# Performance work log

Hardware: AMD Instinct MI355X
Metric: run time of the kernel (lower is better)

Reference implementation:

```python
import jax, jax.numpy as jnp
import numpy as np
import math

D = 768
H = 12
DH = D // H
L = 2
EPS = 1e-12
NEG = -10000.0


def layer_norm(x, w, b):
    u = jnp.mean(x, axis=-1, keepdims=True)
    s = jnp.mean((x - u) ** 2, axis=-1, keepdims=True)
    return w * ((x - u) / jnp.sqrt(s + EPS)) + b


def mha(q_in, k_in, v_in, mask, qw, qb, kw, kb, vw, vb):
    # q_in: (B,Lq,D); k_in/v_in: (B,Lk,D); mask: (B,Lq,Lk) or (B,1,Lk)
    B, Lq, _ = q_in.shape
    def proj(x, w, b):
        y = x @ w.T + b
        return y.reshape(x.shape[0], x.shape[1], H, DH).transpose(0, 2, 1, 3)
    q = proj(q_in, qw, qb)  # (B,H,Lq,DH)
    k = proj(k_in, kw, kb)
    v = proj(v_in, vw, vb)
    scores = jnp.einsum('bhqd,bhkd->bhqk', q, k) / math.sqrt(DH)
    scores = scores + (1.0 - mask[:, None]) * NEG  # additive mask, (B,1,Lq,Lk) broadcast
    probs = jax.nn.softmax(scores, axis=-1)
    ctx = jnp.einsum('bhqk,bhkd->bhqd', probs, v)
    return ctx.transpose(0, 2, 1, 3).reshape(B, Lq, D)


def setup_inputs() -> dict:
    key = jax.random.key(0)
    ks = jax.random.split(key, 8)
    B, Lt, Lv = 8, 1024, 512
    inp = {
        'dec_hidden_states': jax.random.normal(ks[0], (B, Lt, D), jnp.float32),
        'dec_mask': jnp.ones((B, Lt), jnp.float32),
        'enc_outputs': jax.random.normal(ks[1], (B, Lv, D), jnp.float32),
        'enc_mask': jnp.ones((B, Lv), jnp.float32),
    }
    wkeys = jax.random.split(ks[2], 7)
    names = ['sa_qw', 'sa_kw', 'sa_vw', 'ca_qw', 'ca_kw', 'ca_vw', 'out_w']
    for n, k in zip(names, wkeys):
        inp[n] = 0.02 * jax.random.normal(k, (L, D, D), jnp.float32)
    for n in ['sa_qb', 'sa_kb', 'sa_vb', 'ca_qb', 'ca_kb', 'ca_vb', 'out_b', 'n1_b', 'n2_b', 'n3_b']:
        inp[n] = jnp.zeros((L, D), jnp.float32)
    for n in ['n1_w', 'n2_w', 'n3_w']:
        inp[n] = jnp.ones((L, D), jnp.float32)
    return inp


def reference(dec_hidden_states, dec_mask, enc_outputs, enc_mask,
              sa_qw, sa_qb, sa_kw, sa_kb, sa_vw, sa_vb, n1_w, n1_b,
              ca_qw, ca_qb, ca_kw, ca_kb, ca_vw, ca_vb, n2_w, n2_b,
              out_w, out_b, n3_w, n3_b):
    Lt = dec_hidden_states.shape[1]
    causal = jnp.tril(jnp.ones((Lt, Lt), dec_mask.dtype))
    self_mask = dec_mask[:, None, :] * causal[None]        # (B,Lt,Lt)
    cross_mask = enc_mask[:, None, :]                      # (B,1,Lv)

    params = (sa_qw, sa_qb, sa_kw, sa_kb, sa_vw, sa_vb, n1_w, n1_b,
              ca_qw, ca_qb, ca_kw, ca_kb, ca_vw, ca_vb, n2_w, n2_b,
              out_w, out_b, n3_w, n3_b)

    def body(x, p):
        (qw, qb, kw, kb, vw, vb, w1, b1,
         cqw, cqb, ckw, ckb, cvw, cvb, w2, b2,
         ow, ob, w3, b3) = p
        a = mha(x, x, x, self_mask, qw, qb, kw, kb, vw, vb)
        x1 = layer_norm(a + x, w1, b1)
        c = mha(x1, enc_outputs, enc_outputs, cross_mask, cqw, cqb, ckw, ckb, cvw, cvb)
        x2 = layer_norm(x1 + c, w2, b2)
        # BertOutput called with (x2, x2): LN(dense(x2) + x2)
        y = layer_norm(x2 @ ow.T + ob + x2, w3, b3)
        return y, None

    out, _ = jax.lax.scan(body, dec_hidden_states, params)
    return out
```

## Files before the change

kernel.cpp:

```cpp
#include <hip/hip_runtime.h>
#include <hip/hip_bf16.h>

#define DMODEL 768
#define NH 12
#define DH 64
#define NEGC -10000.0f

#define AS1 __attribute__((address_space(1)))
#define AS3 __attribute__((address_space(3)))

typedef __bf16 bf16_t;
typedef __bf16 bf16x8 __attribute__((ext_vector_type(8)));
typedef __bf16 bf16x4 __attribute__((ext_vector_type(4)));
typedef float f32x4 __attribute__((ext_vector_type(4)));
typedef unsigned int u32x2 __attribute__((ext_vector_type(2)));

__device__ __forceinline__ f32x4 mfma16(bf16x8 a, bf16x8 b, f32x4 c) {
    return __builtin_amdgcn_mfma_f32_16x16x32_bf16(a, b, c, 0, 0, 0);
}

__device__ __forceinline__ void gl_lds16(const bf16_t* g, void* l) {
    __builtin_amdgcn_global_load_lds((const AS1 void*)g, (AS3 void*)l, 16, 0, 0);
}

__global__ void probe_kernel(const unsigned int* m, int* flag) {
    *flag = (m[0] == 0x3F803F80u) ? 1 : 0;
}

__device__ __forceinline__ void cvt_group(const void* src, bf16_t* dst, int g, int isbf16) {
    if (isbf16) {
        ((bf16x8*)dst)[g] = ((const bf16x8*)src)[g];
    } else {
        const float* s = (const float*)src + (size_t)g * 8;
        bf16x8 v;
#pragma unroll
        for (int i = 0; i < 8; i++) v[i] = (bf16_t)s[i];
        ((bf16x8*)dst)[g] = v;
    }
}

__global__ __launch_bounds__(256) void cvt_kernel(const void* src, bf16_t* dst,
                                                  const int* flag, int n) {
    int g = blockIdx.x * 256 + threadIdx.x;
    if (g * 8 >= n) return;
    cvt_group(src, dst, g, *flag);
}

__global__ __launch_bounds__(256) void cvt7_kernel(
    const void* s0, const void* s1, const void* s2, const void* s3,
    const void* s4, const void* s5, const void* s6,
    bf16_t* dst, const int* flag)
{
    const void* srcs[7] = {s0, s1, s2, s3, s4, s5, s6};
    const void* src = srcs[blockIdx.y];
    bf16_t* d = dst + (size_t)blockIdx.y * 1179648;
    int g = blockIdx.x * 256 + threadIdx.x;
    cvt_group(src, d, g, *flag);
}

__global__ __launch_bounds__(256) void cvt13_kernel(
    const void* s0, const void* s1, const void* s2, const void* s3,
    const void* s4, const void* s5, const void* s6, const void* s7,
    const void* s8, const void* s9, const void* s10, const void* s11,
    const void* s12, bf16_t* dst, const int* flag)
{
    const void* srcs[13] = {s0, s1, s2, s3, s4, s5, s6, s7, s8, s9, s10, s11, s12};
    const void* src = srcs[blockIdx.x];
    bf16_t* d = dst + (size_t)blockIdx.x * 1536;
    int g = threadIdx.x;
    if (g >= 192) return;
    cvt_group(src, d, g, *flag);
}

__global__ __launch_bounds__(512, 2) void gemm256x128_kernel(
    const bf16_t* __restrict__ X0, const bf16_t* __restrict__ X1,
    const bf16_t* __restrict__ X2,
    const bf16_t* __restrict__ W0, const bf16_t* __restrict__ W1,
    const bf16_t* __restrict__ W2,
    const bf16_t* __restrict__ B0, const bf16_t* __restrict__ B1,
    const bf16_t* __restrict__ B2,
    bf16_t* __restrict__ O0, bf16_t* __restrict__ O1, bf16_t* __restrict__ O2,
    int nx, int ny0, int ny1, int ny2, int nz, int vz, int lkShift)
{
    __shared__ __attribute__((aligned(16))) bf16_t alds[3][256 * 64];
    __shared__ __attribute__((aligned(16))) bf16_t blds[3][128 * 64];

    const int tid  = threadIdx.x;
    const int lane = tid & 63;
    const int w    = tid >> 6;
    const int r    = lane & 15;
    const int q4   = lane >> 4;

    const int id     = blockIdx.x;
    const int xcd    = id & 7;
    const int slot   = id >> 3;
    const int planes = nx * nz;
    const int band   = xcd + 8 * (slot / planes);
    const int p      = slot % planes;
    const int z      = p / nx;
    const int bx     = p - z * nx;

    const int nyz = (z == 0) ? ny0 : ((z == 1) ? ny1 : ny2);
    if (band >= nyz) return;

    const int row0 = band * 256;
    const int col0 = bx * 128;
    const int wr   = w >> 1;
    const int wc   = w & 1;
    const int wrow = wr * 64;
    const int wcol = wc * 64;

    const bf16_t* X    = (z == 0) ? X0 : ((z == 1) ? X1 : X2);
    const bf16_t* W    = (z == 0) ? W0 : ((z == 1) ? W1 : W2);
    const bf16_t* bias = (z == 0) ? B0 : ((z == 1) ? B1 : B2);
    bf16_t*       out  = (z == 0) ? O0 : ((z == 1) ? O1 : O2);
    const int     mode = (z == vz) ? 1 : 0;

    const f32x4 zero4 = {0.f, 0.f, 0.f, 0.f};
    f32x4 acc[4][4];
#pragma unroll
    for (int i = 0; i < 4; i++)
#pragma unroll
        for (int j = 0; j < 4; j++) acc[i][j] = zero4;

    const int srowA = w * 32 + (lane >> 3);
    const int srowB = w * 16 + (lane >> 3);
    const int sgcA  = (lane & 7) ^ (srowA & 7);
    const int sgcB  = (lane & 7) ^ (srowB & 7);
    const bf16_t* Xs = X + (size_t)(row0 + srowA) * DMODEL + sgcA * 8;
    const bf16_t* Ws = W + (size_t)(col0 + srowB) * DMODEL + sgcB * 8;

    auto stageH = [&](int buf, int kb, int half) {
#pragma unroll
        for (int j = 0; j < 2; j++)
            gl_lds16(Xs + (size_t)((half * 2 + j) * 8) * DMODEL + kb,
                     (char*)&alds[buf][0] + w * 4096 + (half * 2 + j) * 1024);
        gl_lds16(Ws + (size_t)(half * 8) * DMODEL + kb,
                 (char*)&blds[buf][0] + w * 2048 + half * 1024);
    };

    const int NIT = DMODEL / 64;
    stageH(0, 0, 0);  stageH(0, 0, 1);
    stageH(1, 64, 0); stageH(1, 64, 1);
    for (int i = 0; i < NIT; i++) {
        const int cur = i % 3;
        const int nxt = (i + 2) % 3;
        const int kb2 = (i + 2) * 64;
        const bool dostage = (i + 2) < NIT;

        if (i + 1 < NIT) {
            asm volatile("s_waitcnt vmcnt(6)" ::: "memory");
        } else {
            asm volatile("s_waitcnt vmcnt(0)" ::: "memory");
        }
        __builtin_amdgcn_s_barrier();

        const bf16_t* al = alds[cur];
        const bf16_t* bl = blds[cur];
#pragma unroll
        for (int ks = 0; ks < 2; ks++) {
            bf16x8 af[4], bf[4];
#pragma unroll
            for (int ii = 0; ii < 4; ii++) {
                int rr_ = wrow + ii * 16 + r;
                int pc  = (ks * 4 + q4) ^ (rr_ & 7);
                af[ii] = *(const bf16x8*)&al[rr_ * 64 + pc * 8];
            }
#pragma unroll
            for (int j = 0; j < 4; j++) {
                int cc_ = wcol + j * 16 + r;
                int pc  = (ks * 4 + q4) ^ (cc_ & 7);
                bf[j] = *(const bf16x8*)&bl[cc_ * 64 + pc * 8];
            }
            if (dostage) stageH(nxt, kb2, ks);
            asm volatile("s_waitcnt lgkmcnt(0)" ::: "memory");
            __builtin_amdgcn_s_setprio(1);
#pragma unroll
            for (int ii = 0; ii < 4; ii++)
#pragma unroll
                for (int j = 0; j < 4; j++)
                    acc[ii][j] = mfma16(af[ii], bf[j], acc[ii][j]);
            __builtin_amdgcn_s_setprio(0);
            __builtin_amdgcn_s_barrier();
        }
    }

#pragma unroll
    for (int i = 0; i < 4; i++)
#pragma unroll
        for (int j = 0; j < 4; j++) {
            int gcol = col0 + wcol + j * 16 + r;
            float bv = (float)bias[gcol];
            if (mode == 0) {
#pragma unroll
                for (int rr = 0; rr < 4; rr++) {
                    int grow = row0 + wrow + i * 16 + q4 * 4 + rr;
                    out[(size_t)grow * DMODEL + gcol] = (bf16_t)(acc[i][j][rr] + bv);
                }
            } else {
                int growb = row0 + wrow + i * 16 + q4 * 4;
                int bidx  = growb >> lkShift;
                int t     = growb & ((1 << lkShift) - 1);
                int h     = gcol >> 6;
                int dd    = gcol & 63;
                union { bf16_t h4[4]; u32x2 v; } pk;
#pragma unroll
                for (int rr = 0; rr < 4; rr++)
                    pk.h4[rr] = (bf16_t)(acc[i][j][rr] + bv);
                *reinterpret_cast<u32x2*>(
                    &out[((size_t)((bidx * NH + h) * 64 + dd) << lkShift) + t]) = pk.v;
            }
        }
}

__global__ __launch_bounds__(256, 3) void attn_kernel(
    const bf16_t* Q, const bf16_t* __restrict__ K,
    const bf16_t* __restrict__ Vt, const bf16_t* __restrict__ mask,
    bf16_t* ctx, int Lq, int Lk, int causal)
{
    __shared__ __attribute__((aligned(16))) bf16_t kvlds[2][2][4096];
    __shared__ __attribute__((aligned(16))) bf16_t plds[4][2048];
    const int tid  = threadIdx.x;
    const int lane = tid & 63;
    const int wv   = tid >> 6;
    const int r    = lane & 15;
    const int q4   = lane >> 4;
    const int b    = blockIdx.z;
    const int h    = blockIdx.y;
    const int qblk = (gridDim.x - 1 - blockIdx.x) * 128;
    const int qbase = qblk + wv * 32;

    bf16x8 qf[2][2];
#pragma unroll
    for (int g = 0; g < 2; g++) {
        const bf16_t* Qp = Q + ((size_t)(b * Lq + qbase + g * 16 + r)) * DMODEL
                           + h * DH + q4 * 8;
        qf[g][0] = *(const bf16x8*)(Qp);
        qf[g][1] = *(const bf16x8*)(Qp + 32);
    }
    const bf16_t* Kg = K + ((size_t)b * Lk) * DMODEL + h * DH;
    const bf16_t* Vg = Vt + ((size_t)(b * NH + h) * DH) * Lk;
    const bf16_t* mp = mask + (size_t)b * Lk;

    const f32x4 zero4 = {0.f, 0.f, 0.f, 0.f};
    float psum[2][4] = {{0.f, 0.f, 0.f, 0.f}, {0.f, 0.f, 0.f, 0.f}};
    f32x4 o[2][4];
#pragma unroll
    for (int g = 0; g < 2; g++)
#pragma unroll
        for (int nc = 0; nc < 4; nc++) o[g][nc] = zero4;

    const int nt = causal ? ((qblk >> 6) + 2) : (Lk >> 6);

    auto stage = [&](int buf, int kb) {
#pragma unroll
        for (int j = 0; j < 2; j++) {
            gl_lds16(Kg + (size_t)(kb + wv * 16 + r) * DMODEL + (j * 4 + q4) * 8,
                     &kvlds[buf][0][wv * 1024 + j * 512]);
            gl_lds16(Vg + (size_t)(wv * 16 + r) * Lk + kb + (j * 4 + q4) * 8,
                     &kvlds[buf][1][wv * 1024 + j * 512]);
        }
    };

    stage(0, 0);
    for (int i = 0; i < nt; i++) {
        const int kb  = i << 6;
        const int cur = i & 1;
        asm volatile("s_waitcnt lgkmcnt(0)" ::: "memory");
        __builtin_amdgcn_s_barrier();
        float mb[4];
#pragma unroll
        for (int t = 0; t < 4; t++)
            mb[t] = (1.f - (float)mp[kb + t * 16 + r]) * NEGC;
        if (i + 1 < nt) {
            stage(cur ^ 1, kb + 64);
            asm volatile("s_waitcnt vmcnt(4)" ::: "memory");
        } else {
            asm volatile("s_waitcnt vmcnt(0)" ::: "memory");
        }
        __builtin_amdgcn_s_barrier();

        if (causal && kb > qbase + 31) continue;

        const bf16_t* kl = kvlds[cur][0];
        const bf16_t* vl = kvlds[cur][1];
        f32x4 s[2][4];
#pragma unroll
        for (int t = 0; t < 4; t++) {
            bf16x8 k0 = *(const bf16x8*)&kl[t * 1024 + lane * 8];
            bf16x8 k1 = *(const bf16x8*)&kl[t * 1024 + 512 + lane * 8];
            s[0][t] = mfma16(qf[0][1], k1, mfma16(qf[0][0], k0, zero4));
            s[1][t] = mfma16(qf[1][1], k1, mfma16(qf[1][0], k0, zero4));
        }
        const bool needMask = causal && (kb + 63 > qbase);
        if (needMask) {
#pragma unroll
            for (int g = 0; g < 2; g++)
#pragma unroll
                for (int t = 0; t < 4; t++)
#pragma unroll
                    for (int rr = 0; rr < 4; rr++) {
                        float f = s[g][t][rr] * 0.125f + mb[t];
                        float pv = __expf(f);
                        if (kb + t * 16 + r > qbase + g * 16 + q4 * 4 + rr) pv = 0.f;
                        psum[g][rr] += pv;
                        plds[wv][g * 1024 + (t * 2 + (r >> 3)) * 128 +
                                 (q4 * 4 + rr) * 8 + (r & 7)] = (bf16_t)pv;
                    }
        } else {
#pragma unroll
            for (int g = 0; g < 2; g++)
#pragma unroll
                for (int t = 0; t < 4; t++)
#pragma unroll
                    for (int rr = 0; rr < 4; rr++) {
                        float f = s[g][t][rr] * 0.125f + mb[t];
                        float pv = __expf(f);
                        psum[g][rr] += pv;
                        plds[wv][g * 1024 + (t * 2 + (r >> 3)) * 128 +
                                 (q4 * 4 + rr) * 8 + (r & 7)] = (bf16_t)pv;
                    }
        }
        bf16x8 pa[2][2];
#pragma unroll
        for (int g = 0; g < 2; g++) {
            pa[g][0] = *(const bf16x8*)&plds[wv][g * 1024 + lane * 8];
            pa[g][1] = *(const bf16x8*)&plds[wv][g * 1024 + 512 + lane * 8];
        }
#pragma unroll
        for (int nc = 0; nc < 4; nc++) {
            bf16x8 v0 = *(const bf16x8*)&vl[nc * 1024 + lane * 8];
            bf16x8 v1 = *(const bf16x8*)&vl[nc * 1024 + 512 + lane * 8];
            o[0][nc] = mfma16(pa[0][1], v1, mfma16(pa[0][0], v0, o[0][nc]));
            o[1][nc] = mfma16(pa[1][1], v1, mfma16(pa[1][0], v0, o[1][nc]));
        }
    }

#pragma unroll
    for (int g = 0; g < 2; g++)
#pragma unroll
        for (int rr = 0; rr < 4; rr++) {
            psum[g][rr] += __shfl_xor(psum[g][rr], 1, 64);
            psum[g][rr] += __shfl_xor(psum[g][rr], 2, 64);
            psum[g][rr] += __shfl_xor(psum[g][rr], 4, 64);
            psum[g][rr] += __shfl_xor(psum[g][rr], 8, 64);
        }
#pragma unroll
    for (int g = 0; g < 2; g++)
#pragma unroll
        for (int nc = 0; nc < 4; nc++)
#pragma unroll
            for (int rr = 0; rr < 4; rr++) {
                int qi = qbase + g * 16 + q4 * 4 + rr;
                ctx[((size_t)(b * Lq + qi)) * DMODEL + h * DH + nc * 16 + r] =
                    (bf16_t)(o[g][nc][rr] / psum[g][rr]);
            }
}

__global__ __launch_bounds__(256) void ln_kernel(
    const bf16_t* __restrict__ a, const bf16_t* __restrict__ res,
    const bf16_t* __restrict__ w, const bf16_t* __restrict__ b,
    void* out, int fin, const int* __restrict__ flag)
{
    const int lane = threadIdx.x & 63;
    const int wv   = threadIdx.x >> 6;
    const int row  = blockIdx.x * 4 + wv;
    const bf16_t* ap = a + (size_t)row * DMODEL;
    const bf16_t* rp = res + (size_t)row * DMODEL;
    const int outf32 = fin && (*flag == 0);

    float v[12];
#pragma unroll
    for (int p = 0; p < 3; p++) {
        int e = (p * 64 + lane) * 4;
        bf16x4 av = *(const bf16x4*)&ap[e];
        bf16x4 rv = *(const bf16x4*)&rp[e];
#pragma unroll
        for (int j = 0; j < 4; j++)
            v[p * 4 + j] = (float)av[j] + (float)rv[j];
    }
    float s = 0.f;
#pragma unroll
    for (int k = 0; k < 12; k++) s += v[k];
#pragma unroll
    for (int m = 1; m < 64; m <<= 1) s += __shfl_xor(s, m, 64);
    const float u = s * (1.0f / DMODEL);
    float s2 = 0.f;
#pragma unroll
    for (int k = 0; k < 12; k++) { float d = v[k] - u; s2 += d * d; }
#pragma unroll
    for (int m = 1; m < 64; m <<= 1) s2 += __shfl_xor(s2, m, 64);
    const float rstd = rsqrtf(s2 * (1.0f / DMODEL) + 1e-12f);

#pragma unroll
    for (int p = 0; p < 3; p++) {
        int e = (p * 64 + lane) * 4;
        bf16x4 wv4 = *(const bf16x4*)&w[e];
        bf16x4 bv4 = *(const bf16x4*)&b[e];
        float y[4];
#pragma unroll
        for (int j = 0; j < 4; j++)
            y[j] = ((v[p * 4 + j] - u) * rstd) * (float)wv4[j] + (float)bv4[j];
        if (outf32) {
            f32x4 o4 = {y[0], y[1], y[2], y[3]};
            *(f32x4*)&((float*)out)[(size_t)row * DMODEL + e] = o4;
        } else {
            bf16x4 o4;
#pragma unroll
            for (int j = 0; j < 4; j++) o4[j] = (bf16_t)y[j];
            *(bf16x4*)&((bf16_t*)out)[(size_t)row * DMODEL + e] = o4;
        }
    }
}

extern "C" void kernel_launch(void* const* d_in, const int* in_sizes, int n_in,
                              void* d_out, int out_size, void* d_ws, size_t ws_size,
                              hipStream_t stream)
{
    const int B = 8, Lt = 1024, Lv = 512;
    const size_t A = (size_t)B * Lt * DMODEL;
    const size_t E = (size_t)B * Lv * DMODEL;
    const size_t WT = 2 * (size_t)DMODEL * DMODEL;
    const int WSZ = DMODEL * DMODEL;

    char* p = (char*)d_ws;
    int* flagp = (int*)p;            p += 64;
    bf16_t* cdec = (bf16_t*)p;       p += A * 2;
    bf16_t* cenc = (bf16_t*)p;       p += E * 2;
    bf16_t* cdm  = (bf16_t*)p;       p += (size_t)B * Lt * 2;
    bf16_t* cem  = (bf16_t*)p;       p += (size_t)B * Lv * 2;
    bf16_t* cw   = (bf16_t*)p;       p += 7 * WT * 2;
    bf16_t* cb   = (bf16_t*)p;       p += 13 * 1536 * 2;
    bf16_t* b0   = (bf16_t*)p;       p += A * 2;
    bf16_t* b1   = (bf16_t*)p;       p += A * 2;
    bf16_t* b2   = (bf16_t*)p;       p += A * 2;
    bf16_t* dob  = (bf16_t*)d_out;

    const bf16_t* sa_qw = cw + 0 * WT, * sa_kw = cw + 1 * WT, * sa_vw = cw + 2 * WT;
    const bf16_t* ca_qw = cw + 3 * WT, * ca_kw = cw + 4 * WT, * ca_vw = cw + 5 * WT;
    const bf16_t* out_w = cw + 6 * WT;
    const bf16_t* sa_qb = cb + 0 * 1536, * sa_kb = cb + 1 * 1536, * sa_vb = cb + 2 * 1536;
    const bf16_t* ca_qb = cb + 3 * 1536, * ca_kb = cb + 4 * 1536, * ca_vb = cb + 5 * 1536;
    const bf16_t* out_b = cb + 6 * 1536;
    const bf16_t* n1_b  = cb + 7 * 1536, * n2_b = cb + 8 * 1536, * n3_b = cb + 9 * 1536;
    const bf16_t* n1_w  = cb + 10 * 1536, * n2_w = cb + 11 * 1536, * n3_w = cb + 12 * 1536;

    probe_kernel<<<1, 1, 0, stream>>>((const unsigned int*)d_in[1], flagp);
    cvt_kernel<<<dim3((unsigned)(A / 2048)), 256, 0, stream>>>(d_in[0], cdec, flagp, (int)A);
    cvt_kernel<<<dim3((unsigned)(E / 2048)), 256, 0, stream>>>(d_in[2], cenc, flagp, (int)E);
    cvt_kernel<<<dim3(4),  256, 0, stream>>>(d_in[1], cdm, flagp, B * Lt);
    cvt_kernel<<<dim3(2),  256, 0, stream>>>(d_in[3], cem, flagp, B * Lv);
    cvt7_kernel<<<dim3(576, 7), 256, 0, stream>>>(
        d_in[4], d_in[5], d_in[6], d_in[7], d_in[8], d_in[9], d_in[10], cw, flagp);
    cvt13_kernel<<<dim3(13), 256, 0, stream>>>(
        d_in[11], d_in[12], d_in[13], d_in[14], d_in[15], d_in[16], d_in[17],
        d_in[18], d_in[19], d_in[20], d_in[21], d_in[22], d_in[23], cb, flagp);

    dim3 blk256(256);
    dim3 blk512(512);
    dim3 gQKV(6 * 32 * 3);
    dim3 gCrs(6 * 32 * 3);
    dim3 gOut(6 * 32);
    dim3 gAttn(Lt / 128, NH, B);
    dim3 gLN(B * Lt / 4);

    for (int l = 0; l < 2; l++) {
        const bf16_t* xin = (l == 0) ? cdec : dob;
        gemm256x128_kernel<<<gQKV, blk512, 0, stream>>>(
            xin, xin, xin,
            sa_qw + l * WSZ, sa_kw + l * WSZ, sa_vw + l * WSZ,
            sa_qb + l * DMODEL, sa_kb + l * DMODEL, sa_vb + l * DMODEL,
            b0, b1, b2, 6, 32, 32, 32, 3, 2, 10);
        attn_kernel<<<gAttn, blk256, 0, stream>>>(b0, b1, b2, cdm, b0, Lt, Lt, 1);
        ln_kernel<<<gLN, blk256, 0, stream>>>(b0, xin, n1_w + l * DMODEL, n1_b + l * DMODEL, b0, 0, flagp);
        gemm256x128_kernel<<<gCrs, blk512, 0, stream>>>(
            b0, cenc, cenc,
            ca_qw + l * WSZ, ca_kw + l * WSZ, ca_vw + l * WSZ,
            ca_qb + l * DMODEL, ca_kb + l * DMODEL, ca_vb + l * DMODEL,
            b1, b2, dob, 6, 32, 16, 16, 3, 2, 9);
        attn_kernel<<<gAttn, blk256, 0, stream>>>(b1, b2, dob, cem, b1, Lt, Lv, 0);
        ln_kernel<<<gLN, blk256, 0, stream>>>(b1, b0, n2_w + l * DMODEL, n2_b + l * DMODEL, b1, 0, flagp);
        gemm256x128_kernel<<<gOut, blk512, 0, stream>>>(
            b1, b1, b1,
            out_w + l * WSZ, out_w, out_w,
            out_b + l * DMODEL, out_b, out_b,
            b2, b2, b2, 6, 32, 32, 32, 1, -1, 0);
        ln_kernel<<<gLN, blk256, 0, stream>>>(b2, b1, n3_w + l * DMODEL, n3_b + l * DMODEL, dob, (l == 1) ? 1 : 0, flagp);
    }
}
```

Baseline: 593.9 us.

## Transpose QK^T MFMA output so each lane packs probabilities into vector LDS stores

The QK^T MFMA operands are swapped so each lane holds four consecutive key columns for one query row. The lane can then convert pairs with v_cvt_pk_bf16_f32 and write 8-byte packed stores to the P LDS buffer instead of scalar 2-byte stores. Mask values are loaded as bf16x4 vectors, and the row-sum reduction changes to two cross-lane xors plus shuffles to redistribute. s_setprio raises wave priority around the MFMA blocks. The new index mapping must match the layout the PV MFMA reads, which is a correctness risk.

```diff
diff --git a/kernel.cpp b/kernel.cpp
--- a/kernel.cpp
+++ b/kernel.cpp
@@ -243,7 +243,7 @@
     const bf16_t* mp = mask + (size_t)b * Lk;
 
     const f32x4 zero4 = {0.f, 0.f, 0.f, 0.f};
-    float psum[2][4] = {{0.f, 0.f, 0.f, 0.f}, {0.f, 0.f, 0.f, 0.f}};
+    float psum[2][2] = {{0.f, 0.f}, {0.f, 0.f}};
     f32x4 o[2][4];
 #pragma unroll
     for (int g = 0; g < 2; g++)
@@ -268,10 +268,14 @@
         const int cur = i & 1;
         asm volatile("s_waitcnt lgkmcnt(0)" ::: "memory");
         __builtin_amdgcn_s_barrier();
-        float mb[4];
-#pragma unroll
-        for (int t = 0; t < 4; t++)
-            mb[t] = (1.f - (float)mp[kb + t * 16 + r]) * NEGC;
+        float mbf[4][4];
+#pragma unroll
+        for (int t = 0; t < 4; t++) {
+            bf16x4 mv = *(const bf16x4*)&mp[kb + t * 16 + q4 * 4];
+#pragma unroll
+            for (int rr = 0; rr < 4; rr++)
+                mbf[t][rr] = (1.f - (float)mv[rr]) * NEGC;
+        }
         if (i + 1 < nt) {
             stage(cur ^ 1, kb + 64);
             asm volatile("s_waitcnt vmcnt(4)" ::: "memory");
@@ -285,41 +289,46 @@
         const bf16_t* kl = kvlds[cur][0];
         const bf16_t* vl = kvlds[cur][1];
         f32x4 s[2][4];
+        __builtin_amdgcn_s_setprio(1);
 #pragma unroll
         for (int t = 0; t < 4; t++) {
             bf16x8 k0 = *(const bf16x8*)&kl[t * 1024 + lane * 8];
             bf16x8 k1 = *(const bf16x8*)&kl[t * 1024 + 512 + lane * 8];
-            s[0][t] = mfma16(qf[0][1], k1, mfma16(qf[0][0], k0, zero4));
-            s[1][t] = mfma16(qf[1][1], k1, mfma16(qf[1][0], k0, zero4));
-        }
+            s[0][t] = mfma16(k1, qf[0][1], mfma16(k0, qf[0][0], zero4));
+            s[1][t] = mfma16(k1, qf[1][1], mfma16(k0, qf[1][0], zero4));
+        }
+        __builtin_amdgcn_s_setprio(0);
+
         const bool needMask = causal && (kb + 63 > qbase);
-        if (needMask) {
-#pragma unroll
-            for (int g = 0; g < 2; g++)
-#pragma unroll
-                for (int t = 0; t < 4; t++)
+#pragma unroll
+        for (int g = 0; g < 2; g++) {
+#pragma unroll
+            for (int t = 0; t < 4; t++) {
+                float pv[4];
+                if (needMask) {
 #pragma unroll
                     for (int rr = 0; rr < 4; rr++) {
-                        float f = s[g][t][rr] * 0.125f + mb[t];
-                        float pv = __expf(f);
-                        if (kb + t * 16 + r > qbase + g * 16 + q4 * 4 + rr) pv = 0.f;
-                        psum[g][rr] += pv;
-                        plds[wv][g * 1024 + (t * 2 + (r >> 3)) * 128 +
-                                 (q4 * 4 + rr) * 8 + (r & 7)] = (bf16_t)pv;
+                        float f = s[g][t][rr] * 0.125f + mbf[t][rr];
+                        float e = __expf(f);
+                        if (kb + t * 16 + q4 * 4 + rr > qbase + g * 16 + r) e = 0.f;
+                        pv[rr] = e;
                     }
-        } else {
-#pragma unroll
-            for (int g = 0; g < 2; g++)
-#pragma unroll
-                for (int t = 0; t < 4; t++)
+                } else {
 #pragma unroll
                     for (int rr = 0; rr < 4; rr++) {
-                        float f = s[g][t][rr] * 0.125f + mb[t];
-                        float pv = __expf(f);
-                        psum[g][rr] += pv;
-                        plds[wv][g * 1024 + (t * 2 + (r >> 3)) * 128 +
-                                 (q4 * 4 + rr) * 8 + (r & 7)] = (bf16_t)pv;
+                        float f = s[g][t][rr] * 0.125f + mbf[t][rr];
+                        pv[rr] = __expf(f);
                     }
+                }
+                psum[g][0] += pv[0] + pv[1];
+                psum[g][1] += pv[2] + pv[3];
+                unsigned int lo, hi;
+                asm("v_cvt_pk_bf16_f32 %0, %1, %2" : "=v"(lo) : "v"(pv[0]), "v"(pv[1]));
+                asm("v_cvt_pk_bf16_f32 %0, %1, %2" : "=v"(hi) : "v"(pv[2]), "v"(pv[3]));
+                u32x2 pk = {lo, hi};
+                *(u32x2*)&plds[wv][g * 1024 + (t * 2 + (q4 >> 1)) * 128 +
+                                   r * 8 + (q4 & 1) * 4] = pk;
+            }
         }
         bf16x8 pa[2][2];
 #pragma unroll
@@ -327,6 +336,7 @@
             pa[g][0] = *(const bf16x8*)&plds[wv][g * 1024 + lane * 8];
             pa[g][1] = *(const bf16x8*)&plds[wv][g * 1024 + 512 + lane * 8];
         }
+        __builtin_amdgcn_s_setprio(1);
 #pragma unroll
         for (int nc = 0; nc < 4; nc++) {
             bf16x8 v0 = *(const bf16x8*)&vl[nc * 1024 + lane * 8];
@@ -334,27 +344,27 @@
             o[0][nc] = mfma16(pa[0][1], v1, mfma16(pa[0][0], v0, o[0][nc]));
             o[1][nc] = mfma16(pa[1][1], v1, mfma16(pa[1][0], v0, o[1][nc]));
         }
-    }
-
-#pragma unroll
-    for (int g = 0; g < 2; g++)
-#pragma unroll
-        for (int rr = 0; rr < 4; rr++) {
-            psum[g][rr] += __shfl_xor(psum[g][rr], 1, 64);
-            psum[g][rr] += __shfl_xor(psum[g][rr], 2, 64);
-            psum[g][rr] += __shfl_xor(psum[g][rr], 4, 64);
-            psum[g][rr] += __shfl_xor(psum[g][rr], 8, 64);
-        }
-#pragma unroll
-    for (int g = 0; g < 2; g++)
+        __builtin_amdgcn_s_setprio(0);
+    }
+
+#pragma unroll
+    for (int g = 0; g < 2; g++) {
+        float ps = psum[g][0] + psum[g][1];
+        ps += __shfl_xor(ps, 16, 64);
+        ps += __shfl_xor(ps, 32, 64);
+        float pso[4];
+#pragma unroll
+        for (int rr = 0; rr < 4; rr++)
+            pso[rr] = __shfl(ps, q4 * 4 + rr, 64);
 #pragma unroll
         for (int nc = 0; nc < 4; nc++)
 #pragma unroll
             for (int rr = 0; rr < 4; rr++) {
                 int qi = qbase + g * 16 + q4 * 4 + rr;
                 ctx[((size_t)(b * Lq + qi)) * DMODEL + h * DH + nc * 16 + r] =
-                    (bf16_t)(o[g][nc][rr] / psum[g][rr]);
+                    (bf16_t)(o[g][nc][rr] / pso[rr]);
             }
+    }
 }
 
 __global__ __launch_bounds__(256) void ln_kernel(
```

New measurement: 602.3 us. Within noise of the previous version (+1.4%).

## Use 256x256 tiles for QKV projection GEMMs with asymmetric A/B buffering

Applied to the files above, without the earlier changes.

The fused QKV and cross-attention projection GEMMs move from 256x128 to 256x256 output tiles. Each wave now computes a 64x128 sub-tile with 32 accumulators, which halves how often the activation rows are reloaded per output column. LDS is rearranged so A uses three buffers and B two, with the B and A prefetches split across the two k-steps. The output GEMM keeps the old 256x128 kernel in a simplified single-matrix form. Costs are higher register pressure, fewer blocks (288 instead of 576) and possibly less overlap on B loads.

```diff
diff --git a/kernel.cpp b/kernel.cpp
--- a/kernel.cpp
+++ b/kernel.cpp
@@ -72,7 +72,7 @@
     cvt_group(src, d, g, *flag);
 }
 
-__global__ __launch_bounds__(512, 2) void gemm256x128_kernel(
+__global__ __launch_bounds__(512, 2) void gemm256sq_kernel(
     const bf16_t* __restrict__ X0, const bf16_t* __restrict__ X1,
     const bf16_t* __restrict__ X2,
     const bf16_t* __restrict__ W0, const bf16_t* __restrict__ W1,
@@ -83,7 +83,7 @@
     int nx, int ny0, int ny1, int ny2, int nz, int vz, int lkShift)
 {
     __shared__ __attribute__((aligned(16))) bf16_t alds[3][256 * 64];
-    __shared__ __attribute__((aligned(16))) bf16_t blds[3][128 * 64];
+    __shared__ __attribute__((aligned(16))) bf16_t blds[2][256 * 64];
 
     const int tid  = threadIdx.x;
     const int lane = tid & 63;
@@ -104,11 +104,11 @@
     if (band >= nyz) return;
 
     const int row0 = band * 256;
-    const int col0 = bx * 128;
+    const int col0 = bx * 256;
     const int wr   = w >> 1;
     const int wc   = w & 1;
     const int wrow = wr * 64;
-    const int wcol = wc * 64;
+    const int wcol = wc * 128;
 
     const bf16_t* X    = (z == 0) ? X0 : ((z == 1) ? X1 : X2);
     const bf16_t* W    = (z == 0) ? W0 : ((z == 1) ? W1 : W2);
@@ -117,49 +117,48 @@
     const int     mode = (z == vz) ? 1 : 0;
 
     const f32x4 zero4 = {0.f, 0.f, 0.f, 0.f};
-    f32x4 acc[4][4];
+    f32x4 acc[4][8];
 #pragma unroll
     for (int i = 0; i < 4; i++)
 #pragma unroll
-        for (int j = 0; j < 4; j++) acc[i][j] = zero4;
-
-    const int srowA = w * 32 + (lane >> 3);
-    const int srowB = w * 16 + (lane >> 3);
-    const int sgcA  = (lane & 7) ^ (srowA & 7);
-    const int sgcB  = (lane & 7) ^ (srowB & 7);
-    const bf16_t* Xs = X + (size_t)(row0 + srowA) * DMODEL + sgcA * 8;
-    const bf16_t* Ws = W + (size_t)(col0 + srowB) * DMODEL + sgcB * 8;
-
-    auto stageH = [&](int buf, int kb, int half) {
-#pragma unroll
-        for (int j = 0; j < 2; j++)
-            gl_lds16(Xs + (size_t)((half * 2 + j) * 8) * DMODEL + kb,
-                     (char*)&alds[buf][0] + w * 4096 + (half * 2 + j) * 1024);
-        gl_lds16(Ws + (size_t)(half * 8) * DMODEL + kb,
-                 (char*)&blds[buf][0] + w * 2048 + half * 1024);
+        for (int j = 0; j < 8; j++) acc[i][j] = zero4;
+
+    const int srow = w * 32 + (lane >> 3);
+    const int sgc  = (lane & 7) ^ (srow & 7);
+    const bf16_t* Xs = X + (size_t)(row0 + srow) * DMODEL + sgc * 8;
+    const bf16_t* Ws = W + (size_t)(col0 + srow) * DMODEL + sgc * 8;
+
+    auto stageA = [&](int buf, int kb) {
+#pragma unroll
+        for (int j = 0; j < 4; j++)
+            gl_lds16(Xs + (size_t)(j * 8) * DMODEL + kb,
+                     (char*)&alds[buf][0] + w * 4096 + j * 1024);
     };
+    auto stageB = [&](int buf, int kb) {
+#pragma unroll
+        for (int j = 0; j < 4; j++)
+            gl_lds16(Ws + (size_t)(j * 8) * DMODEL + kb,
+                     (char*)&blds[buf][0] + w * 4096 + j * 1024);
+    };
 
     const int NIT = DMODEL / 64;
-    stageH(0, 0, 0);  stageH(0, 0, 1);
-    stageH(1, 64, 0); stageH(1, 64, 1);
+    stageA(0, 0); stageB(0, 0); stageA(1, 64);
     for (int i = 0; i < NIT; i++) {
-        const int cur = i % 3;
-        const int nxt = (i + 2) % 3;
-        const int kb2 = (i + 2) * 64;
-        const bool dostage = (i + 2) < NIT;
+        const int curA = i % 3;
+        const int curB = i & 1;
 
         if (i + 1 < NIT) {
-            asm volatile("s_waitcnt vmcnt(6)" ::: "memory");
+            asm volatile("s_waitcnt vmcnt(4)" ::: "memory");
         } else {
             asm volatile("s_waitcnt vmcnt(0)" ::: "memory");
         }
         __builtin_amdgcn_s_barrier();
 
-        const bf16_t* al = alds[cur];
-        const bf16_t* bl = blds[cur];
+        const bf16_t* al = alds[curA];
+        const bf16_t* bl = blds[curB];
 #pragma unroll
         for (int ks = 0; ks < 2; ks++) {
-            bf16x8 af[4], bf[4];
+            bf16x8 af[4], bf[8];
 #pragma unroll
             for (int ii = 0; ii < 4; ii++) {
                 int rr_ = wrow + ii * 16 + r;
@@ -167,18 +166,19 @@
                 af[ii] = *(const bf16x8*)&al[rr_ * 64 + pc * 8];
             }
 #pragma unroll
-            for (int j = 0; j < 4; j++) {
+            for (int j = 0; j < 8; j++) {
                 int cc_ = wcol + j * 16 + r;
                 int pc  = (ks * 4 + q4) ^ (cc_ & 7);
                 bf[j] = *(const bf16x8*)&bl[cc_ * 64 + pc * 8];
             }
-            if (dostage) stageH(nxt, kb2, ks);
+            if (ks == 0) { if (i + 1 < NIT) stageB((i + 1) & 1, (i + 1) * 64); }
+            else         { if (i + 2 < NIT) stageA((i + 2) % 3, (i + 2) * 64); }
             asm volatile("s_waitcnt lgkmcnt(0)" ::: "memory");
             __builtin_amdgcn_s_setprio(1);
 #pragma unroll
             for (int ii = 0; ii < 4; ii++)
 #pragma unroll
-                for (int j = 0; j < 4; j++)
+                for (int j = 0; j < 8; j++)
                     acc[ii][j] = mfma16(af[ii], bf[j], acc[ii][j]);
             __builtin_amdgcn_s_setprio(0);
             __builtin_amdgcn_s_barrier();
@@ -188,7 +188,7 @@
 #pragma unroll
     for (int i = 0; i < 4; i++)
 #pragma unroll
-        for (int j = 0; j < 4; j++) {
+        for (int j = 0; j < 8; j++) {
             int gcol = col0 + wcol + j * 16 + r;
             float bv = (float)bias[gcol];
             if (mode == 0) {
@@ -209,6 +209,117 @@
                     pk.h4[rr] = (bf16_t)(acc[i][j][rr] + bv);
                 *reinterpret_cast<u32x2*>(
                     &out[((size_t)((bidx * NH + h) * 64 + dd) << lkShift) + t]) = pk.v;
+            }
+        }
+}
+
+__global__ __launch_bounds__(512, 2) void gemm256x128_kernel(
+    const bf16_t* __restrict__ X,
+    const bf16_t* __restrict__ W,
+    const bf16_t* __restrict__ Bb,
+    bf16_t* __restrict__ out,
+    int nx, int ny)
+{
+    __shared__ __attribute__((aligned(16))) bf16_t alds[3][256 * 64];
+    __shared__ __attribute__((aligned(16))) bf16_t blds[3][128 * 64];
+
+    const int tid  = threadIdx.x;
+    const int lane = tid & 63;
+    const int w    = tid >> 6;
+    const int r    = lane & 15;
+    const int q4   = lane >> 4;
+
+    const int id     = blockIdx.x;
+    const int xcd    = id & 7;
+    const int slot   = id >> 3;
+    const int band   = xcd + 8 * (slot / nx);
+    const int bx     = slot % nx;
+    const int row0   = band * 256;
+    const int col0   = bx * 128;
+    const int wr     = w >> 1;
+    const int wc     = w & 1;
+    const int wrow   = wr * 64;
+    const int wcol   = wc * 64;
+
+    const f32x4 zero4 = {0.f, 0.f, 0.f, 0.f};
+    f32x4 acc[4][4];
+#pragma unroll
+    for (int i = 0; i < 4; i++)
+#pragma unroll
+        for (int j = 0; j < 4; j++) acc[i][j] = zero4;
+
+    const int srowA = w * 32 + (lane >> 3);
+    const int srowB = w * 16 + (lane >> 3);
+    const int sgcA  = (lane & 7) ^ (srowA & 7);
+    const int sgcB  = (lane & 7) ^ (srowB & 7);
+    const bf16_t* Xs = X + (size_t)(row0 + srowA) * DMODEL + sgcA * 8;
+    const bf16_t* Ws = W + (size_t)(col0 + srowB) * DMODEL + sgcB * 8;
+
+    auto stageH = [&](int buf, int kb, int half) {
+#pragma unroll
+        for (int j = 0; j < 2; j++)
+            gl_lds16(Xs + (size_t)((half * 2 + j) * 8) * DMODEL + kb,
+                     (char*)&alds[buf][0] + w * 4096 + (half * 2 + j) * 1024);
+        gl_lds16(Ws + (size_t)(half * 8) * DMODEL + kb,
+                 (char*)&blds[buf][0] + w * 2048 + half * 1024);
+    };
+
+    const int NIT = DMODEL / 64;
+    stageH(0, 0, 0);  stageH(0, 0, 1);
+    stageH(1, 64, 0); stageH(1, 64, 1);
+    for (int i = 0; i < NIT; i++) {
+        const int cur = i % 3;
+        const int nxt = (i + 2) % 3;
+        const int kb2 = (i + 2) * 64;
+        const bool dostage = (i + 2) < NIT;
+
+        if (i + 1 < NIT) {
+            asm volatile("s_waitcnt vmcnt(6)" ::: "memory");
+        } else {
+            asm volatile("s_waitcnt vmcnt(0)" ::: "memory");
+        }
+        __builtin_amdgcn_s_barrier();
+
+        const bf16_t* al = alds[cur];
+        const bf16_t* bl = blds[cur];
+#pragma unroll
+        for (int ks = 0; ks < 2; ks++) {
+            bf16x8 af[4], bf[4];
+#pragma unroll
+            for (int ii = 0; ii < 4; ii++) {
+                int rr_ = wrow + ii * 16 + r;
+                int pc  = (ks * 4 + q4) ^ (rr_ & 7);
+                af[ii] = *(const bf16x8*)&al[rr_ * 64 + pc * 8];
+            }
+#pragma unroll
+            for (int j = 0; j < 4; j++) {
+                int cc_ = wcol + j * 16 + r;
+                int pc  = (ks * 4 + q4) ^ (cc_ & 7);
+                bf[j] = *(const bf16x8*)&bl[cc_ * 64 + pc * 8];
+            }
+            if (dostage) stageH(nxt, kb2, ks);
+            asm volatile("s_waitcnt lgkmcnt(0)" ::: "memory");
+            __builtin_amdgcn_s_setprio(1);
+#pragma unroll
+            for (int ii = 0; ii < 4; ii++)
+#pragma unroll
+                for (int j = 0; j < 4; j++)
+                    acc[ii][j] = mfma16(af[ii], bf[j], acc[ii][j]);
+            __builtin_amdgcn_s_setprio(0);
+            __builtin_amdgcn_s_barrier();
+        }
+    }
+
+#pragma unroll
+    for (int i = 0; i < 4; i++)
+#pragma unroll
+        for (int j = 0; j < 4; j++) {
+            int gcol = col0 + wcol + j * 16 + r;
+            float bv = (float)Bb[gcol];
+#pragma unroll
+            for (int rr = 0; rr < 4; rr++) {
+                int grow = row0 + wrow + i * 16 + q4 * 4 + rr;
+                out[(size_t)grow * DMODEL + gcol] = (bf16_t)(acc[i][j][rr] + bv);
             }
         }
 }
@@ -458,33 +569,30 @@
 
     dim3 blk256(256);
     dim3 blk512(512);
-    dim3 gQKV(6 * 32 * 3);
-    dim3 gCrs(6 * 32 * 3);
+    dim3 gQKV(3 * 32 * 3);
+    dim3 gCrs(3 * 32 * 3);
     dim3 gOut(6 * 32);
     dim3 gAttn(Lt / 128, NH, B);
     dim3 gLN(B * Lt / 4);
 
     for (int l = 0; l < 2; l++) {
         const bf16_t* xin = (l == 0) ? cdec : dob;
-        gemm256x128_kernel<<<gQKV, blk512, 0, stream>>>(
+        gemm256sq_kernel<<<gQKV, blk512, 0, stream>>>(
             xin, xin, xin,
             sa_qw + l * WSZ, sa_kw + l * WSZ, sa_vw + l * WSZ,
             sa_qb + l * DMODEL, sa_kb + l * DMODEL, sa_vb + l * DMODEL,
-            b0, b1, b2, 6, 32, 32, 32, 3, 2, 10);
+            b0, b1, b2, 3, 32, 32, 32, 3, 2, 10);
         attn_kernel<<<gAttn, blk256, 0, stream>>>(b0, b1, b2, cdm, b0, Lt, Lt, 1);
         ln_kernel<<<gLN, blk256, 0, stream>>>(b0, xin, n1_w + l * DMODEL, n1_b + l * DMODEL, b0, 0, flagp);
-        gemm256x128_kernel<<<gCrs, blk512, 0, stream>>>(
+        gemm256sq_kernel<<<gCrs, blk512, 0, stream>>>(
             b0, cenc, cenc,
             ca_qw + l * WSZ, ca_kw + l * WSZ, ca_vw + l * WSZ,
             ca_qb + l * DMODEL, ca_kb + l * DMODEL, ca_vb + l * DMODEL,
-            b1, b2, dob, 6, 32, 16, 16, 3, 2, 9);
+            b1, b2, dob, 3, 32, 16, 16, 3, 2, 9);
         attn_kernel<<<gAttn, blk256, 0, stream>>>(b1, b2, dob, cem, b1, Lt, Lv, 0);
         ln_kernel<<<gLN, blk256, 0, stream>>>(b1, b0, n2_w + l * DMODEL, n2_b + l * DMODEL, b1, 0, flagp);
         gemm256x128_kernel<<<gOut, blk512, 0, stream>>>(
-            b1, b1, b1,
-            out_w + l * WSZ, out_w, out_w,
-            out_b + l * DMODEL, out_b, out_b,
-            b2, b2, b2, 6, 32, 32, 32, 1, -1, 0);
+            b1, out_w + l * WSZ, out_b + l * DMODEL, b2, 6, 32);
         ln_kernel<<<gLN, blk256, 0, stream>>>(b2, b1, n3_w + l * DMODEL, n3_b + l * DMODEL, dob, (l == 1) ? 1 : 0, flagp);
     }
 }
```

Result: no change. 597.1 us (+0.5%).
